# Kernel optimization log

Hardware: AMD Instinct MI355X
Metric: run time of the kernel (lower is better)

## Reference

```python
import jax, jax.numpy as jnp
import numpy as np

B, S, H, I, E, TOPK = 2, 2048, 1024, 2048, 8, 2


def setup_inputs() -> dict:
    key = jax.random.key(0)
    ks = jax.random.split(key, 6)
    return {
        "x": jax.random.normal(ks[0], (B, S, H), dtype=jnp.float32),
        "expert_indices": jax.random.randint(ks[1], (B, S, TOPK), 0, E, dtype=jnp.int64),
        "expert_weights": jax.random.uniform(ks[2], (B, S, TOPK), dtype=jnp.float32),
        "gate_proj": jax.random.normal(ks[3], (E, I, H), dtype=jnp.float32) * 0.02,
        "up_proj": jax.random.normal(ks[4], (E, I, H), dtype=jnp.float32) * 0.02,
        "down_proj": jax.random.normal(ks[5], (E, H, I), dtype=jnp.float32) * 0.02,
    }


def reference(x, expert_indices, expert_weights, gate_proj, up_proj, down_proj):
    # x: [B,S,H]; expert_indices/weights: [B,S,K]; gate/up: [E,I,H]; down: [E,H,I]
    b, s, h = x.shape
    e = gate_proj.shape[0]
    xf = x.reshape(-1, h)                      # [T,H]
    t = xf.shape[0]
    idx = expert_indices.reshape(t, -1)        # [T,K]
    w = expert_weights.reshape(t, -1)          # [T,K]
    # Combine per-(token,slot) weights into a per-(token,expert) weight matrix.
    # Identical math to the per-expert index_add_ in the torch module.
    we = jnp.zeros((t, e), dtype=x.dtype).at[jnp.arange(t)[:, None], idx].add(w)  # [T,E]
    gate = jax.nn.silu(jnp.einsum('th,eih->tei', xf, gate_proj))  # [T,E,I]
    up = jnp.einsum('th,eih->tei', xf, up_proj)                   # [T,E,I]
    out_e = jnp.einsum('tei,ehi->teh', gate * up, down_proj)      # [T,E,H]
    out = jnp.einsum('te,teh->th', we, out_e)                     # [T,H]
    return out.reshape(b, s, h)
```

## Files before the change

kernel.cpp:

```cpp
#include <hip/hip_runtime.h>


#define H_DIM 1024
#define I_DIM 2048
#define N_EXP 8
#define N_TOK 4096
#define N_ENT 8192
#define CAP   9216

typedef __attribute__((ext_vector_type(8))) short bhalf8;
typedef __attribute__((ext_vector_type(4))) float floatx4;

__device__ __forceinline__ unsigned short f2bf(float f) {
  unsigned int u = __float_as_uint(f);
  u += 0x7fffu + ((u >> 16) & 1u);
  return (unsigned short)(u >> 16);
}

__device__ __forceinline__ unsigned int pkbf(float a, float b) {
  unsigned int ua = __float_as_uint(a) + 0x8000u;
  unsigned int ub = __float_as_uint(b) + 0x8000u;
  return __builtin_amdgcn_perm(ub, ua, 0x07060302u);
}

__device__ __forceinline__ void ld16(const void* g, void* l) {
  __builtin_amdgcn_global_load_lds(
      (const __attribute__((address_space(1))) unsigned int*)g,
      (__attribute__((address_space(3))) unsigned int*)l, 16, 0, 0);
}

__global__ __launch_bounds__(256) void route_kernel(
    const int* __restrict__ idx, const float* __restrict__ wts,
    int* __restrict__ perm, float* __restrict__ pw, int* __restrict__ inv,
    int* __restrict__ counts, int* __restrict__ poff)
{
  __shared__ int cnt[N_EXP], cur[N_EXP], off[N_EXP];
  const int t = threadIdx.x;
  if (t < N_EXP) { cnt[t] = 0; cur[t] = 0; }
  __syncthreads();
  for (int i = t; i < N_ENT; i += 256) atomicAdd(&cnt[idx[i] & 7], 1);
  __syncthreads();
  if (t == 0) {
    int o = 0;
    for (int e = 0; e < N_EXP; e++) {
      off[e] = o; counts[e] = cnt[e]; poff[e] = o;
      o += ((cnt[e] + 127) >> 7) << 7;
    }
  }
  __syncthreads();
  for (int i = t; i < N_ENT; i += 256) {
    int e = idx[i] & 7;
    int p = atomicAdd(&cur[e], 1);
    int pos = off[e] + p;
    perm[pos] = i >> 1;
    pw[pos] = wts[i];
    inv[i] = pos;
  }
}

__global__ __launch_bounds__(256) void cast_x_kernel(
    const float* __restrict__ s, unsigned short* __restrict__ d)
{
  int i = (blockIdx.x * 256 + threadIdx.x) * 8;
  const float4* sp = (const float4*)(s + i);
  float4 a = sp[0], b = sp[1];
  bhalf8 o;
  o[0] = (short)f2bf(a.x); o[1] = (short)f2bf(a.y); o[2] = (short)f2bf(a.z); o[3] = (short)f2bf(a.w);
  o[4] = (short)f2bf(b.x); o[5] = (short)f2bf(b.y); o[6] = (short)f2bf(b.z); o[7] = (short)f2bf(b.w);
  *(bhalf8*)(d + i) = o;
}

__global__ __launch_bounds__(512, 4) void gemm1_kernel(
    const unsigned short* __restrict__ xb,
    const float* __restrict__ gw,
    const float* __restrict__ uw,
    const int* __restrict__ perm,
    const int* __restrict__ counts,
    const int* __restrict__ poff,
    unsigned short* __restrict__ act)
{
  const int e = blockIdx.z;
  const int Ne = counts[e];
  const int mt = blockIdx.y;
  if (mt * 256 >= Ne) return;
  const int NeR = ((Ne + 127) >> 7) << 7;
  const int base = poff[e];
  const int n0 = blockIdx.x * 64;

  __shared__ __align__(16) unsigned short As[256 * 64];
  __shared__ __align__(16) unsigned short Bgs[64 * 64];
  __shared__ __align__(16) unsigned short Bus[64 * 64];

  const int tid = threadIdx.x;
  const int lane = tid & 63;
  const int w = tid >> 6;
  const int wmi = w >> 1;
  const int wnj = w & 1;
  const int i3 = lane >> 3, i7 = lane & 7;
  const int swc = (i7 ^ i3) * 8;

  const unsigned short* pA[4]; unsigned short* lA[4];
#pragma unroll
  for (int t = 0; t < 4; t++) {
    int rloc = w * 32 + t * 8 + i3;
    int rr = mt * 256 + rloc; rr = rr < Ne ? rr : Ne - 1;
    pA[t] = xb + (size_t)perm[base + rr] * H_DIM + swc;
    lA[t] = &As[(w * 32 + t * 8) * 64];
  }
  const int nlocB = w * 8 + i3;
  const size_t wb = (size_t)e * (I_DIM * H_DIM) + (size_t)(n0 + nlocB) * H_DIM + i7 * 8;
  const float* pg = gw + wb;
  const float* pu = uw + wb;
  unsigned short* lBg = &Bgs[(i7 * 64 + nlocB) * 8];
  unsigned short* lBu = &Bus[(i7 * 64 + nlocB) * 8];

  floatx4 zero = {0.f, 0.f, 0.f, 0.f};
  floatx4 accg[4][2], accu[4][2];
#pragma unroll
  for (int i = 0; i < 4; i++)
#pragma unroll
    for (int j = 0; j < 2; j++) { accg[i][j] = zero; accu[i][j] = zero; }

  const int quad = lane >> 4, lm = lane & 15;
  const int s7 = lm & 7;

  float4 g0 = *(const float4*)(pg);
  float4 g1 = *(const float4*)(pg + 4);
  float4 u0 = *(const float4*)(pu);
  float4 u1 = *(const float4*)(pu + 4);

  for (int k0 = 0; k0 < H_DIM; k0 += 64) {
    __syncthreads();
#pragma unroll
    for (int t = 0; t < 4; t++) ld16(pA[t] + k0, lA[t]);
    *(uint4*)lBg = make_uint4(pkbf(g0.x, g0.y), pkbf(g0.z, g0.w),
                              pkbf(g1.x, g1.y), pkbf(g1.z, g1.w));
    *(uint4*)lBu = make_uint4(pkbf(u0.x, u0.y), pkbf(u0.z, u0.w),
                              pkbf(u1.x, u1.y), pkbf(u1.z, u1.w));
    __syncthreads();
    if (k0 + 64 < H_DIM) {
      g0 = *(const float4*)(pg + k0 + 64);
      g1 = *(const float4*)(pg + k0 + 68);
      u0 = *(const float4*)(pu + k0 + 64);
      u1 = *(const float4*)(pu + k0 + 68);
    }
#pragma unroll
    for (int kk = 0; kk < 2; kk++) {
      const int kq = kk * 4 + quad;
      const int ko = (kq ^ s7) * 8;
      bhalf8 a[4], bg[2], bu[2];
#pragma unroll
      for (int i = 0; i < 4; i++)
        a[i] = *(const bhalf8*)&As[(wmi * 64 + i * 16 + lm) * 64 + ko];
#pragma unroll
      for (int j = 0; j < 2; j++) {
        bg[j] = *(const bhalf8*)&Bgs[(kq * 64 + wnj * 32 + j * 16 + lm) * 8];
        bu[j] = *(const bhalf8*)&Bus[(kq * 64 + wnj * 32 + j * 16 + lm) * 8];
      }
#pragma unroll
      for (int i = 0; i < 4; i++)
#pragma unroll
        for (int j = 0; j < 2; j++) {
          accg[i][j] = __builtin_amdgcn_mfma_f32_16x16x32_bf16(a[i], bg[j], accg[i][j], 0, 0, 0);
          accu[i][j] = __builtin_amdgcn_mfma_f32_16x16x32_bf16(a[i], bu[j], accu[i][j], 0, 0, 0);
        }
    }
  }

#pragma unroll
  for (int i = 0; i < 4; i++) {
#pragma unroll
    for (int r = 0; r < 4; r++) {
      int row = mt * 256 + wmi * 64 + i * 16 + quad * 4 + r;
      if (row < NeR) {
        size_t rowoff = (size_t)(base + row) * I_DIM;
#pragma unroll
        for (int j = 0; j < 2; j++) {
          int col = n0 + wnj * 32 + j * 16 + lm;
          float g = accg[i][j][r];
          float u = accu[i][j][r];
          float h = (g / (1.f + __expf(-g))) * u;
          act[rowoff + col] = (unsigned short)f2bf(h);
        }
      }
    }
  }
}

__global__ __launch_bounds__(512, 4) void gemm2_kernel(
    const unsigned short* __restrict__ act,
    const float* __restrict__ dw,
    const float* __restrict__ pw,
    const int* __restrict__ counts,
    const int* __restrict__ poff,
    float* __restrict__ ent)
{
  const int e = blockIdx.z;
  const int Ne = counts[e];
  const int mt = blockIdx.y;
  if (mt * 256 >= Ne) return;
  const int NeR = ((Ne + 127) >> 7) << 7;
  const int base = poff[e];
  const int n0 = (blockIdx.x & 7) * 128;
  const int k_lo = (blockIdx.x >> 3) * (I_DIM / 2);

  __shared__ __align__(16) unsigned short As[256 * 64];
  __shared__ __align__(16) unsigned short Bs[128 * 64];

  const int tid = threadIdx.x;
  const int lane = tid & 63;
  const int w = tid >> 6;
  const int wmi = w >> 1, wnj = w & 1;
  const int i3 = lane >> 3, i7 = lane & 7;
  const int swc = (i7 ^ i3) * 8;

  const unsigned short* pA[4]; unsigned short* lA[4];
#pragma unroll
  for (int t = 0; t < 4; t++) {
    int rloc = w * 32 + t * 8 + i3;
    int rr = mt * 256 + rloc; rr = rr < NeR ? rr : NeR - 1;
    pA[t] = act + (size_t)(base + rr) * I_DIM + k_lo + swc;
    lA[t] = &As[(w * 32 + t * 8) * 64];
  }
  const float* pB[2]; unsigned short* lB[2];
#pragma unroll
  for (int t = 0; t < 2; t++) {
    int rloc = w * 16 + t * 8 + i3;
    pB[t] = dw + (size_t)e * (H_DIM * I_DIM) + (size_t)(n0 + rloc) * I_DIM + k_lo + i7 * 8;
    lB[t] = &Bs[(i7 * 128 + rloc) * 8];
  }

  floatx4 zero = {0.f, 0.f, 0.f, 0.f};
  floatx4 acc[4][4];
#pragma unroll
  for (int i = 0; i < 4; i++)
#pragma unroll
    for (int j = 0; j < 4; j++) acc[i][j] = zero;

  const int quad = lane >> 4, lm = lane & 15;
  const int s7 = lm & 7;

  float4 b00 = *(const float4*)(pB[0]);
  float4 b01 = *(const float4*)(pB[0] + 4);
  float4 b10 = *(const float4*)(pB[1]);
  float4 b11 = *(const float4*)(pB[1] + 4);

  for (int k0 = 0; k0 < I_DIM / 2; k0 += 64) {
    __syncthreads();
#pragma unroll
    for (int t = 0; t < 4; t++) ld16(pA[t] + k0, lA[t]);
    *(uint4*)lB[0] = make_uint4(pkbf(b00.x, b00.y), pkbf(b00.z, b00.w),
                                pkbf(b01.x, b01.y), pkbf(b01.z, b01.w));
    *(uint4*)lB[1] = make_uint4(pkbf(b10.x, b10.y), pkbf(b10.z, b10.w),
                                pkbf(b11.x, b11.y), pkbf(b11.z, b11.w));
    __syncthreads();
    if (k0 + 64 < I_DIM / 2) {
      b00 = *(const float4*)(pB[0] + k0 + 64);
      b01 = *(const float4*)(pB[0] + k0 + 68);
      b10 = *(const float4*)(pB[1] + k0 + 64);
      b11 = *(const float4*)(pB[1] + k0 + 68);
    }
#pragma unroll
    for (int kk = 0; kk < 2; kk++) {
      const int kq = kk * 4 + quad;
      const int ko = (kq ^ s7) * 8;
      bhalf8 a[4], b[4];
#pragma unroll
      for (int i = 0; i < 4; i++)
        a[i] = *(const bhalf8*)&As[(wmi * 64 + i * 16 + lm) * 64 + ko];
#pragma unroll
      for (int j = 0; j < 4; j++)
        b[j] = *(const bhalf8*)&Bs[(kq * 128 + wnj * 64 + j * 16 + lm) * 8];
#pragma unroll
      for (int i = 0; i < 4; i++)
#pragma unroll
        for (int j = 0; j < 4; j++)
          acc[i][j] = __builtin_amdgcn_mfma_f32_16x16x32_bf16(a[i], b[j], acc[i][j], 0, 0, 0);
    }
  }

  float* enth = ent + (size_t)(blockIdx.x >> 3) * CAP * H_DIM;
#pragma unroll
  for (int i = 0; i < 4; i++) {
#pragma unroll
    for (int r = 0; r < 4; r++) {
      int row = mt * 256 + wmi * 64 + i * 16 + quad * 4 + r;
      if (row < Ne) {
        float wt = pw[base + row];
        float* orow = enth + (size_t)(base + row) * H_DIM;
#pragma unroll
        for (int j = 0; j < 4; j++) {
          int col = n0 + wnj * 64 + j * 16 + lm;
          orow[col] = wt * acc[i][j][r];
        }
      }
    }
  }
}

__global__ __launch_bounds__(256) void combine_kernel(
    const float* __restrict__ ent, const int* __restrict__ inv,
    float* __restrict__ out)
{
  const int t = blockIdx.x;
  const int p0 = inv[2 * t], p1 = inv[2 * t + 1];
  const float4* r0 = (const float4*)(ent + (size_t)p0 * H_DIM);
  const float4* r1 = (const float4*)(ent + (size_t)p1 * H_DIM);
  const float4* r2 = (const float4*)(ent + (size_t)(CAP + p0) * H_DIM);
  const float4* r3 = (const float4*)(ent + (size_t)(CAP + p1) * H_DIM);
  float4 a = r0[threadIdx.x], b = r1[threadIdx.x];
  float4 c = r2[threadIdx.x], d = r3[threadIdx.x];
  float4 o = {a.x + b.x + c.x + d.x, a.y + b.y + c.y + d.y,
              a.z + b.z + c.z + d.z, a.w + b.w + c.w + d.w};
  ((float4*)(out + (size_t)t * H_DIM))[threadIdx.x] = o;
}

extern "C" void kernel_launch(void* const* d_in, const int* in_sizes, int n_in,
                              void* d_out, int out_size, void* d_ws, size_t ws_size,
                              hipStream_t stream) {
  const float* x    = (const float*)d_in[0];
  const int*   idx  = (const int*)d_in[1];
  const float* wts  = (const float*)d_in[2];
  const float* gate = (const float*)d_in[3];
  const float* up   = (const float*)d_in[4];
  const float* down = (const float*)d_in[5];
  float* out = (float*)d_out;
  char* ws = (char*)d_ws;

  float*          ent = (float*)(ws + 0);
  unsigned short* act = (unsigned short*)(ws + 75497472);
  unsigned short* xb  = (unsigned short*)(ws + 113246208);
  int*   perm   = (int*)(ws + 121634816);
  float* pw     = (float*)(ws + 121671680);
  int*   inv    = (int*)(ws + 121708544);
  int*   counts = (int*)(ws + 121741312);
  int*   poff   = (int*)(ws + 121741376);

  route_kernel<<<1, 256, 0, stream>>>(idx, wts, perm, pw, inv, counts, poff);

  cast_x_kernel<<<(N_TOK * H_DIM) / (256 * 8), 256, 0, stream>>>(x, xb);

  gemm1_kernel<<<dim3(I_DIM / 64, 32, N_EXP), 512, 0, stream>>>(
      xb, gate, up, perm, counts, poff, act);

  gemm2_kernel<<<dim3(16, 32, N_EXP), 512, 0, stream>>>(
      act, down, pw, counts, poff, ent);

  combine_kernel<<<N_TOK, 256, 0, stream>>>(ent, inv, out);
}
```

Baseline: 416.4 us.

## Pre-cast expert weights to bf16 and stream them into LDS directly

Adds separate cast passes that convert the gate, up and down weight tensors to bf16 in workspace on every call. The two GEMM kernels then load weight tiles with global_load_lds into a swizzled LDS layout, the same way they already load activations. This removes the per-tile fp32 register loads and in-kernel packing, and halves the bytes each GEMM reads for weights. In exchange it adds about 200MB of extra fp32 reads plus 100MB of bf16 writes per call, and drops the register prefetch of the next weight tile. The gate and up bf16 copies reuse the ent buffer region, which is only safe because gemm2 writes ent after gemm1 has finished reading them.

```diff
diff --git a/kernel.cpp b/kernel.cpp
--- a/kernel.cpp
+++ b/kernel.cpp
@@ -15,12 +15,6 @@
   unsigned int u = __float_as_uint(f);
   u += 0x7fffu + ((u >> 16) & 1u);
   return (unsigned short)(u >> 16);
-}
-
-__device__ __forceinline__ unsigned int pkbf(float a, float b) {
-  unsigned int ua = __float_as_uint(a) + 0x8000u;
-  unsigned int ub = __float_as_uint(b) + 0x8000u;
-  return __builtin_amdgcn_perm(ub, ua, 0x07060302u);
 }
 
 __device__ __forceinline__ void ld16(const void* g, void* l) {
@@ -58,10 +52,10 @@
   }
 }
 
-__global__ __launch_bounds__(256) void cast_x_kernel(
+__global__ __launch_bounds__(256) void cast_kernel(
     const float* __restrict__ s, unsigned short* __restrict__ d)
 {
-  int i = (blockIdx.x * 256 + threadIdx.x) * 8;
+  size_t i = ((size_t)blockIdx.x * 256 + threadIdx.x) * 8;
   const float4* sp = (const float4*)(s + i);
   float4 a = sp[0], b = sp[1];
   bhalf8 o;
@@ -72,8 +66,8 @@
 
 __global__ __launch_bounds__(512, 4) void gemm1_kernel(
     const unsigned short* __restrict__ xb,
-    const float* __restrict__ gw,
-    const float* __restrict__ uw,
+    const unsigned short* __restrict__ gwb,
+    const unsigned short* __restrict__ uwb,
     const int* __restrict__ perm,
     const int* __restrict__ counts,
     const int* __restrict__ poff,
@@ -107,12 +101,11 @@
     pA[t] = xb + (size_t)perm[base + rr] * H_DIM + swc;
     lA[t] = &As[(w * 32 + t * 8) * 64];
   }
-  const int nlocB = w * 8 + i3;
-  const size_t wb = (size_t)e * (I_DIM * H_DIM) + (size_t)(n0 + nlocB) * H_DIM + i7 * 8;
-  const float* pg = gw + wb;
-  const float* pu = uw + wb;
-  unsigned short* lBg = &Bgs[(i7 * 64 + nlocB) * 8];
-  unsigned short* lBu = &Bus[(i7 * 64 + nlocB) * 8];
+  const size_t wb = (size_t)e * (I_DIM * H_DIM) + (size_t)(n0 + w * 8 + i3) * H_DIM + swc;
+  const unsigned short* pBg = gwb + wb;
+  const unsigned short* pBu = uwb + wb;
+  unsigned short* lBg = &Bgs[(w * 8) * 64];
+  unsigned short* lBu = &Bus[(w * 8) * 64];
 
   floatx4 zero = {0.f, 0.f, 0.f, 0.f};
   floatx4 accg[4][2], accu[4][2];
@@ -124,26 +117,13 @@
   const int quad = lane >> 4, lm = lane & 15;
   const int s7 = lm & 7;
 
-  float4 g0 = *(const float4*)(pg);
-  float4 g1 = *(const float4*)(pg + 4);
-  float4 u0 = *(const float4*)(pu);
-  float4 u1 = *(const float4*)(pu + 4);
-
   for (int k0 = 0; k0 < H_DIM; k0 += 64) {
     __syncthreads();
 #pragma unroll
     for (int t = 0; t < 4; t++) ld16(pA[t] + k0, lA[t]);
-    *(uint4*)lBg = make_uint4(pkbf(g0.x, g0.y), pkbf(g0.z, g0.w),
-                              pkbf(g1.x, g1.y), pkbf(g1.z, g1.w));
-    *(uint4*)lBu = make_uint4(pkbf(u0.x, u0.y), pkbf(u0.z, u0.w),
-                              pkbf(u1.x, u1.y), pkbf(u1.z, u1.w));
+    ld16(pBg + k0, lBg);
+    ld16(pBu + k0, lBu);
     __syncthreads();
-    if (k0 + 64 < H_DIM) {
-      g0 = *(const float4*)(pg + k0 + 64);
-      g1 = *(const float4*)(pg + k0 + 68);
-      u0 = *(const float4*)(pu + k0 + 64);
-      u1 = *(const float4*)(pu + k0 + 68);
-    }
 #pragma unroll
     for (int kk = 0; kk < 2; kk++) {
       const int kq = kk * 4 + quad;
@@ -154,8 +134,8 @@
         a[i] = *(const bhalf8*)&As[(wmi * 64 + i * 16 + lm) * 64 + ko];
 #pragma unroll
       for (int j = 0; j < 2; j++) {
-        bg[j] = *(const bhalf8*)&Bgs[(kq * 64 + wnj * 32 + j * 16 + lm) * 8];
-        bu[j] = *(const bhalf8*)&Bus[(kq * 64 + wnj * 32 + j * 16 + lm) * 8];
+        bg[j] = *(const bhalf8*)&Bgs[(wnj * 32 + j * 16 + lm) * 64 + ko];
+        bu[j] = *(const bhalf8*)&Bus[(wnj * 32 + j * 16 + lm) * 64 + ko];
       }
 #pragma unroll
       for (int i = 0; i < 4; i++)
@@ -189,7 +169,7 @@
 
 __global__ __launch_bounds__(512, 4) void gemm2_kernel(
     const unsigned short* __restrict__ act,
-    const float* __restrict__ dw,
+    const unsigned short* __restrict__ dwb,
     const float* __restrict__ pw,
     const int* __restrict__ counts,
     const int* __restrict__ poff,
@@ -222,12 +202,12 @@
     pA[t] = act + (size_t)(base + rr) * I_DIM + k_lo + swc;
     lA[t] = &As[(w * 32 + t * 8) * 64];
   }
-  const float* pB[2]; unsigned short* lB[2];
+  const unsigned short* pB[2]; unsigned short* lB[2];
 #pragma unroll
   for (int t = 0; t < 2; t++) {
     int rloc = w * 16 + t * 8 + i3;
-    pB[t] = dw + (size_t)e * (H_DIM * I_DIM) + (size_t)(n0 + rloc) * I_DIM + k_lo + i7 * 8;
-    lB[t] = &Bs[(i7 * 128 + rloc) * 8];
+    pB[t] = dwb + (size_t)e * (H_DIM * I_DIM) + (size_t)(n0 + rloc) * I_DIM + k_lo + swc;
+    lB[t] = &Bs[(w * 16 + t * 8) * 64];
   }
 
   floatx4 zero = {0.f, 0.f, 0.f, 0.f};
@@ -240,26 +220,13 @@
   const int quad = lane >> 4, lm = lane & 15;
   const int s7 = lm & 7;
 
-  float4 b00 = *(const float4*)(pB[0]);
-  float4 b01 = *(const float4*)(pB[0] + 4);
-  float4 b10 = *(const float4*)(pB[1]);
-  float4 b11 = *(const float4*)(pB[1] + 4);
-
   for (int k0 = 0; k0 < I_DIM / 2; k0 += 64) {
     __syncthreads();
 #pragma unroll
     for (int t = 0; t < 4; t++) ld16(pA[t] + k0, lA[t]);
-    *(uint4*)lB[0] = make_uint4(pkbf(b00.x, b00.y), pkbf(b00.z, b00.w),
-                                pkbf(b01.x, b01.y), pkbf(b01.z, b01.w));
-    *(uint4*)lB[1] = make_uint4(pkbf(b10.x, b10.y), pkbf(b10.z, b10.w),
-                                pkbf(b11.x, b11.y), pkbf(b11.z, b11.w));
+#pragma unroll
+    for (int t = 0; t < 2; t++) ld16(pB[t] + k0, lB[t]);
     __syncthreads();
-    if (k0 + 64 < I_DIM / 2) {
-      b00 = *(const float4*)(pB[0] + k0 + 64);
-      b01 = *(const float4*)(pB[0] + k0 + 68);
-      b10 = *(const float4*)(pB[1] + k0 + 64);
-      b11 = *(const float4*)(pB[1] + k0 + 68);
-    }
 #pragma unroll
     for (int kk = 0; kk < 2; kk++) {
       const int kq = kk * 4 + quad;
@@ -270,7 +237,7 @@
         a[i] = *(const bhalf8*)&As[(wmi * 64 + i * 16 + lm) * 64 + ko];
 #pragma unroll
       for (int j = 0; j < 4; j++)
-        b[j] = *(const bhalf8*)&Bs[(kq * 128 + wnj * 64 + j * 16 + lm) * 8];
+        b[j] = *(const bhalf8*)&Bs[(wnj * 64 + j * 16 + lm) * 64 + ko];
 #pragma unroll
       for (int i = 0; i < 4; i++)
 #pragma unroll
@@ -328,23 +295,29 @@
   char* ws = (char*)d_ws;
 
   float*          ent = (float*)(ws + 0);
+  unsigned short* gb  = (unsigned short*)(ws + 0);
+  unsigned short* ub  = (unsigned short*)(ws + 33554432);
   unsigned short* act = (unsigned short*)(ws + 75497472);
   unsigned short* xb  = (unsigned short*)(ws + 113246208);
-  int*   perm   = (int*)(ws + 121634816);
-  float* pw     = (float*)(ws + 121671680);
-  int*   inv    = (int*)(ws + 121708544);
-  int*   counts = (int*)(ws + 121741312);
-  int*   poff   = (int*)(ws + 121741376);
+  unsigned short* db  = (unsigned short*)(ws + 121634816);
+  int*   perm   = (int*)(ws + 155189248);
+  float* pw     = (float*)(ws + 155226112);
+  int*   inv    = (int*)(ws + 155262976);
+  int*   counts = (int*)(ws + 155295744);
+  int*   poff   = (int*)(ws + 155295808);
 
   route_kernel<<<1, 256, 0, stream>>>(idx, wts, perm, pw, inv, counts, poff);
 
-  cast_x_kernel<<<(N_TOK * H_DIM) / (256 * 8), 256, 0, stream>>>(x, xb);
+  cast_kernel<<<(N_TOK * H_DIM) / (256 * 8), 256, 0, stream>>>(x, xb);
+  cast_kernel<<<(N_EXP * I_DIM * H_DIM) / (256 * 8), 256, 0, stream>>>(gate, gb);
+  cast_kernel<<<(N_EXP * I_DIM * H_DIM) / (256 * 8), 256, 0, stream>>>(up, ub);
+  cast_kernel<<<(N_EXP * H_DIM * I_DIM) / (256 * 8), 256, 0, stream>>>(down, db);
 
   gemm1_kernel<<<dim3(I_DIM / 64, 32, N_EXP), 512, 0, stream>>>(
-      xb, gate, up, perm, counts, poff, act);
+      xb, gb, ub, perm, counts, poff, act);
 
   gemm2_kernel<<<dim3(16, 32, N_EXP), 512, 0, stream>>>(
-      act, down, pw, counts, poff, ent);
+      act, db, pw, counts, poff, ent);
 
   combine_kernel<<<N_TOK, 256, 0, stream>>>(ent, inv, out);
 }
```

Result: no change. 421.6 us (+1.3%).
